# Kernel tuning notes

Measured on AMD Instinct MI355X. Metric: run time of the kernel, lower is better.

## Reference

```python
import jax, jax.numpy as jnp
import numpy as np

B, T, C = 2, 2048, 2048
N_HEAD, N_KV_HEAD = 16, 4
HEAD_DIM = C // N_HEAD  # 128
HALF = HEAD_DIM // 2    # 64


def _rms_norm(x):
    # F.rms_norm with no weight: x / sqrt(mean(x^2) + eps), eps = dtype eps
    eps = jnp.finfo(x.dtype).eps
    return x * jax.lax.rsqrt(jnp.mean(x * x, axis=-1, keepdims=True) + eps)


def _rope_apply(x, cos, sin):
    # x: [B, H, T, Hs]; cos/sin: [1, 1, T, Hs/2]
    x1, x2 = x[..., :HALF], x[..., HALF:]
    return jnp.concatenate([x1 * cos - x2 * sin, x1 * sin + x2 * cos], axis=-1)


def setup_inputs() -> dict:
    key = jax.random.key(0)
    ks = jax.random.split(key, 8)
    x = jax.random.normal(ks[0], (B, T, C), dtype=jnp.float32)
    # real RoPE tables (base 10000), shape [1,1,T,HALF]
    inv_freq = 1.0 / (10000.0 ** (np.arange(0, HALF, dtype=np.float32) / HALF))
    t = np.arange(T, dtype=np.float32)
    ang = np.einsum('t,f->tf', t, inv_freq)
    cos = jnp.asarray(np.cos(ang))[None, None]
    sin = jnp.asarray(np.sin(ang))[None, None]
    s = 0.02
    Wq = jax.random.normal(ks[1], (C, N_HEAD * HEAD_DIM), dtype=jnp.float32) * s
    Wk = jax.random.normal(ks[2], (C, N_KV_HEAD * HEAD_DIM), dtype=jnp.float32) * s
    Wv = jax.random.normal(ks[3], (C, N_KV_HEAD * HEAD_DIM), dtype=jnp.float32) * s
    Wo = jax.random.normal(ks[4], (C, C), dtype=jnp.float32) * s
    bo = jnp.zeros((C,), dtype=jnp.float32)
    return {"x": x, "cos": cos, "sin": sin, "Wq": Wq, "Wk": Wk, "Wv": Wv, "Wo": Wo, "bo": bo}


def reference(x, cos, sin, Wq, Wk, Wv, Wo, bo):
    Bq, Tq, Cq = x.shape
    G = N_HEAD // N_KV_HEAD
    # QKV projections (GQA, no bias)
    q = (x @ Wq).reshape(Bq, Tq, N_HEAD, HEAD_DIM)
    k = (x @ Wk).reshape(Bq, Tq, N_KV_HEAD, HEAD_DIM)
    v = (x @ Wv).reshape(Bq, Tq, N_KV_HEAD, HEAD_DIM)
    # QK RMSNorm (over head_dim), then to [B, H, T, Hs]
    q = jnp.transpose(_rms_norm(q), (0, 2, 1, 3))
    k = jnp.transpose(_rms_norm(k), (0, 2, 1, 3))
    v = jnp.transpose(v, (0, 2, 1, 3))
    # RoPE
    q = _rope_apply(q, cos[:, :, :Tq, :], sin[:, :, :Tq, :])
    k = _rope_apply(k, cos[:, :, :Tq, :], sin[:, :, :Tq, :])
    # GQA: repeat kv heads across groups
    k = jnp.repeat(k, G, axis=1)  # [B, H, T, Hs]
    v = jnp.repeat(v, G, axis=1)
    # Causal SDPA
    scale = 1.0 / jnp.sqrt(jnp.asarray(HEAD_DIM, dtype=x.dtype))
    scores = jnp.einsum('bhqd,bhkd->bhqk', q, k) * scale
    causal = jnp.tril(jnp.ones((Tq, Tq), dtype=bool))
    scores = jnp.where(causal, scores, jnp.asarray(-jnp.inf, dtype=scores.dtype))
    attn = jax.nn.softmax(scores, axis=-1)
    y = jnp.einsum('bhqk,bhkd->bhqd', attn, v)
    y = jnp.transpose(y, (0, 2, 1, 3)).reshape(Bq, Tq, Cq)
    return y @ Wo + bo
```

## Files before the change

kernel.cpp:

```cpp
#include <hip/hip_runtime.h>
#include <hip/hip_bf16.h>
#include <math.h>

#define BB 2
#define TT 2048
#define CC 2048
#define NH 16
#define NKV 4
#define HD 128
#define HALF 64
#define MTOT (BB*TT)
#define NQKV (CC + 2*NKV*HD)

typedef unsigned short u16;
typedef __attribute__((ext_vector_type(8))) short bf16x8;
typedef __attribute__((ext_vector_type(4))) float f32x4;

__device__ __forceinline__ u16 f2bf(float f) {
  unsigned u = __float_as_uint(f);
  unsigned r = (u + 0x7FFFu + ((u >> 16) & 1u)) >> 16;
  return (u16)r;
}
__device__ __forceinline__ u16 f2bf_hw(float f) {
  __hip_bfloat16 h = __float2bfloat16(f);
  return *reinterpret_cast<const u16*>(&h);
}
__device__ __forceinline__ float bf2f(u16 v) {
  return __uint_as_float(((unsigned)v) << 16);
}

__device__ __forceinline__ void gl_lds16(const void* g, void* l) {
  __builtin_amdgcn_global_load_lds(
      (const __attribute__((address_space(1))) unsigned int*)g,
      (__attribute__((address_space(3))) unsigned int*)l, 16, 0, 0);
}

__global__ __launch_bounds__(256) void prep(
    const float* __restrict__ x, const float* __restrict__ Wq,
    const float* __restrict__ Wk, const float* __restrict__ Wv,
    const float* __restrict__ Wo, u16* __restrict__ xb,
    u16* __restrict__ Wt, u16* __restrict__ Wot) {
  const int z = blockIdx.z;
  const int tx = threadIdx.x, ty = threadIdx.y;
  if (z == 4) {
    const int tid = ty * 32 + tx;
    const int i = (blockIdx.y * 64 + blockIdx.x) * 256 + tid;
    const float4* s4 = (const float4*)x;
    float4 a = s4[(size_t)i * 2], b = s4[(size_t)i * 2 + 1];
    bf16x8 o;
    o[0] = (short)f2bf(a.x); o[1] = (short)f2bf(a.y);
    o[2] = (short)f2bf(a.z); o[3] = (short)f2bf(a.w);
    o[4] = (short)f2bf(b.x); o[5] = (short)f2bf(b.y);
    o[6] = (short)f2bf(b.z); o[7] = (short)f2bf(b.w);
    ((bf16x8*)xb)[i] = o;
    return;
  }
  const float* W; u16* dst; int N; int row_off;
  if (z == 0)      { W = Wq; dst = Wt;  N = 2048; row_off = 0; }
  else if (z == 1) { W = Wk; dst = Wt;  N = 512;  row_off = 2048; }
  else if (z == 2) { W = Wv; dst = Wt;  N = 512;  row_off = 2560; }
  else             { W = Wo; dst = Wot; N = 2048; row_off = 0; }
  const int n0 = blockIdx.x * 32, k0 = blockIdx.y * 32;
  if (n0 >= N) return;
  __shared__ float tile[32][33];
#pragma unroll
  for (int i = 0; i < 4; ++i)
    tile[ty + 8 * i][tx] = W[(size_t)(k0 + ty + 8 * i) * N + n0 + tx];
  __syncthreads();
#pragma unroll
  for (int i = 0; i < 4; ++i)
    dst[(size_t)(row_off + n0 + ty + 8 * i) * CC + k0 + tx] =
        f2bf(tile[tx][ty + 8 * i]);
}

__global__ __launch_bounds__(512, 2) void gemm_8ph(
    const u16* __restrict__ A, const u16* __restrict__ Bt,
    const float* __restrict__ bias, float* __restrict__ C,
    int M, int N, int K, int out_bf16) {
  __shared__ u16 As[32768];
  __shared__ u16 Bs[32768];
  const int tid = threadIdx.x;
  const int w = tid >> 6, lane = tid & 63;
  const int quad = lane >> 4, lo = lane & 15;
  const int wm = w >> 2, wn = w & 3;
  const int bm = blockIdx.y * 256, bn = blockIdx.x * 256;
  const int NT = K >> 6;

  const u16* agp[2][2]; const u16* bgp[2][2];
#pragma unroll
  for (int h = 0; h < 2; ++h)
#pragma unroll
    for (int j = 0; j < 2; ++j) {
      const unsigned X = (unsigned)h * 16384u +
                         (unsigned)((w * 2 + j) * 64 + lane) * 16u;
      const int row = (int)(X >> 7);
      const int ce = (int)(((X & 127u) ^ (((X >> 7) & 7u) << 4)) >> 1);
      agp[h][j] = A  + (size_t)(bm + row) * K + ce;
      bgp[h][j] = Bt + (size_t)(bn + row) * K + ce;
    }
  char* const lAs = (char*)As;
  char* const lBs = (char*)Bs;
  const int woff = w * 2048;

#define STGA(hh, bufp, kt) do { \
    gl_lds16(agp[hh][0] + (size_t)(kt) * 64, lAs + (bufp) * 32768 + (hh) * 16384 + woff); \
    gl_lds16(agp[hh][1] + (size_t)(kt) * 64, lAs + (bufp) * 32768 + (hh) * 16384 + woff + 1024); \
  } while (0)
#define STGB(hh, bufp, kt) do { \
    gl_lds16(bgp[hh][0] + (size_t)(kt) * 64, lBs + (bufp) * 32768 + (hh) * 16384 + woff); \
    gl_lds16(bgp[hh][1] + (size_t)(kt) * 64, lBs + (bufp) * 32768 + (hh) * 16384 + woff + 1024); \
  } while (0)

  const int sw  = (lo & 7) << 4;
  const int co0 = (quad * 16) ^ sw;
  const int co1 = (64 + quad * 16) ^ sw;
  const int aRB = (wm * 128 + lo) * 128;
  const int bRB = (wn * 64 + lo) * 128;

  f32x4 acc[8][4];
#pragma unroll
  for (int ri = 0; ri < 8; ++ri)
#pragma unroll
    for (int ci = 0; ci < 4; ++ci)
#pragma unroll
      for (int r = 0; r < 4; ++r) acc[ri][ci][r] = 0.f;

  STGA(0, 0, 0); STGA(1, 0, 0); STGB(0, 0, 0); STGB(1, 0, 0);
  STGB(0, 1, 1); STGB(1, 1, 1); STGA(0, 1, 1);
  asm volatile("s_waitcnt vmcnt(6)" ::: "memory");
  __builtin_amdgcn_s_barrier();

  for (int t = 0; t < NT; ++t) {
    const int pa = t & 1;
    const char* Ab = lAs + pa * 32768 + aRB;
    const char* Bb = lBs + pa * 32768 + bRB;
    bf16x8 a[4][2], b0[2][2], b1[2][2];

#pragma unroll
    for (int i = 0; i < 4; ++i) {
      a[i][0] = *(const bf16x8*)(Ab + i * 2048 + co0);
      a[i][1] = *(const bf16x8*)(Ab + i * 2048 + co1);
    }
#pragma unroll
    for (int j = 0; j < 2; ++j) {
      b0[j][0] = *(const bf16x8*)(Bb + j * 2048 + co0);
      b0[j][1] = *(const bf16x8*)(Bb + j * 2048 + co1);
    }
    if (t + 1 < NT) STGA(1, (t + 1) & 1, t + 1);
    __builtin_amdgcn_s_barrier();
    asm volatile("s_waitcnt lgkmcnt(0)");
    __builtin_amdgcn_s_setprio(1);
#pragma unroll
    for (int i = 0; i < 4; ++i)
#pragma unroll
      for (int j = 0; j < 2; ++j) {
        acc[i][j] = __builtin_amdgcn_mfma_f32_16x16x32_bf16(a[i][0], b0[j][0], acc[i][j], 0, 0, 0);
        acc[i][j] = __builtin_amdgcn_mfma_f32_16x16x32_bf16(a[i][1], b0[j][1], acc[i][j], 0, 0, 0);
      }
    __builtin_amdgcn_s_setprio(0);
    __builtin_amdgcn_s_barrier();

#pragma unroll
    for (int j = 0; j < 2; ++j) {
      b1[j][0] = *(const bf16x8*)(Bb + 4096 + j * 2048 + co0);
      b1[j][1] = *(const bf16x8*)(Bb + 4096 + j * 2048 + co1);
    }
    __builtin_amdgcn_s_barrier();
    asm volatile("s_waitcnt lgkmcnt(0)");
    __builtin_amdgcn_s_setprio(1);
#pragma unroll
    for (int i = 0; i < 4; ++i)
#pragma unroll
      for (int j = 0; j < 2; ++j) {
        acc[i][2 + j] = __builtin_amdgcn_mfma_f32_16x16x32_bf16(a[i][0], b1[j][0], acc[i][2 + j], 0, 0, 0);
        acc[i][2 + j] = __builtin_amdgcn_mfma_f32_16x16x32_bf16(a[i][1], b1[j][1], acc[i][2 + j], 0, 0, 0);
      }
    __builtin_amdgcn_s_setprio(0);
    __builtin_amdgcn_s_barrier();

#pragma unroll
    for (int i = 0; i < 4; ++i) {
      a[i][0] = *(const bf16x8*)(Ab + 8192 + i * 2048 + co0);
      a[i][1] = *(const bf16x8*)(Ab + 8192 + i * 2048 + co1);
    }
    if (t + 2 < NT) STGB(0, pa, t + 2);
    __builtin_amdgcn_s_barrier();
    asm volatile("s_waitcnt lgkmcnt(0)");
    __builtin_amdgcn_s_setprio(1);
#pragma unroll
    for (int i = 0; i < 4; ++i)
#pragma unroll
      for (int j = 0; j < 2; ++j) {
        acc[4 + i][2 + j] = __builtin_amdgcn_mfma_f32_16x16x32_bf16(a[i][0], b1[j][0], acc[4 + i][2 + j], 0, 0, 0);
        acc[4 + i][2 + j] = __builtin_amdgcn_mfma_f32_16x16x32_bf16(a[i][1], b1[j][1], acc[4 + i][2 + j], 0, 0, 0);
      }
    __builtin_amdgcn_s_setprio(0);
    __builtin_amdgcn_s_barrier();

    if (t + 2 < NT) { STGB(1, pa, t + 2); STGA(0, pa, t + 2); }
    if (t + 2 < NT)      asm volatile("s_waitcnt vmcnt(6)" ::: "memory");
    else if (t + 1 < NT) asm volatile("s_waitcnt vmcnt(0)" ::: "memory");
    __builtin_amdgcn_s_barrier();
    asm volatile("s_waitcnt lgkmcnt(0)");
    __builtin_amdgcn_s_setprio(1);
#pragma unroll
    for (int i = 0; i < 4; ++i)
#pragma unroll
      for (int j = 0; j < 2; ++j) {
        acc[4 + i][j] = __builtin_amdgcn_mfma_f32_16x16x32_bf16(a[i][0], b0[j][0], acc[4 + i][j], 0, 0, 0);
        acc[4 + i][j] = __builtin_amdgcn_mfma_f32_16x16x32_bf16(a[i][1], b0[j][1], acc[4 + i][j], 0, 0, 0);
      }
    __builtin_amdgcn_s_setprio(0);
    __builtin_amdgcn_s_barrier();
  }
#undef STGA
#undef STGB

  const int rbase = bm + wm * 128;
  const int cbase = bn + wn * 64;
#pragma unroll
  for (int ri = 0; ri < 8; ++ri)
#pragma unroll
    for (int ci = 0; ci < 4; ++ci) {
      const int col = cbase + ci * 16 + lo;
      const float bv = bias ? bias[col] : 0.f;
#pragma unroll
      for (int r = 0; r < 4; ++r) {
        const int row = rbase + ri * 16 + quad * 4 + r;
        const float v = acc[ri][ci][r] + bv;
        if (out_bf16) ((u16*)C)[(size_t)row * N + col] = f2bf(v);
        else          C[(size_t)row * N + col] = v;
      }
    }
}

__global__ __launch_bounds__(512, 2) void gemm_n128(
    const u16* __restrict__ A, const u16* __restrict__ Bt,
    const float* __restrict__ bias, float* __restrict__ C,
    int M, int N, int K, int out_bf16) {
  __shared__ u16 As[32768];
  __shared__ u16 Bs[16384];
  const int tid = threadIdx.x;
  const int w = tid >> 6, lane = tid & 63;
  const int quad = lane >> 4, lo = lane & 15;
  const int wm = w >> 1, wn = w & 1;
  const int bm = blockIdx.y * 256, bn = blockIdx.x * 128;
  const int NT = K >> 6;

  const u16* agp[2][2];
#pragma unroll
  for (int h = 0; h < 2; ++h)
#pragma unroll
    for (int j = 0; j < 2; ++j) {
      const unsigned X = (unsigned)h * 16384u +
                         (unsigned)((w * 2 + j) * 64 + lane) * 16u;
      const int row = (int)(X >> 7);
      const int ce = (int)(((X & 127u) ^ (((X >> 7) & 7u) << 4)) >> 1);
      agp[h][j] = A + (size_t)(bm + row) * K + ce;
    }
  const u16* bgp[2];
#pragma unroll
  for (int j = 0; j < 2; ++j) {
    const unsigned X = (unsigned)((w * 2 + j) * 64 + lane) * 16u;
    const int row = (int)(X >> 7);
    const int ce = (int)(((X & 127u) ^ (((X >> 7) & 7u) << 4)) >> 1);
    bgp[j] = Bt + (size_t)(bn + row) * K + ce;
  }
  char* const lAs = (char*)As;
  char* const lBs = (char*)Bs;
  const int woff = w * 2048;

#define STGA_(hh, bufp, kt) do { \
    gl_lds16(agp[hh][0] + (size_t)(kt) * 64, lAs + (bufp) * 32768 + (hh) * 16384 + woff); \
    gl_lds16(agp[hh][1] + (size_t)(kt) * 64, lAs + (bufp) * 32768 + (hh) * 16384 + woff + 1024); \
  } while (0)
#define STGB_(bufp, kt) do { \
    gl_lds16(bgp[0] + (size_t)(kt) * 64, lBs + (bufp) * 16384 + woff); \
    gl_lds16(bgp[1] + (size_t)(kt) * 64, lBs + (bufp) * 16384 + woff + 1024); \
  } while (0)

  const int sw  = (lo & 7) << 4;
  const int co0 = (quad * 16) ^ sw;
  const int co1 = (64 + quad * 16) ^ sw;
  const int aRB = (wm * 64 + lo) * 128;
  const int bRB = (wn * 64 + lo) * 128;

  f32x4 acc[4][4];
#pragma unroll
  for (int i = 0; i < 4; ++i)
#pragma unroll
    for (int ci = 0; ci < 4; ++ci)
#pragma unroll
      for (int r = 0; r < 4; ++r) acc[i][ci][r] = 0.f;

  STGA_(0, 0, 0); STGA_(1, 0, 0); STGB_(0, 0);
  STGB_(1, 1); STGA_(0, 1, 1);
  asm volatile("s_waitcnt vmcnt(4)" ::: "memory");
  __builtin_amdgcn_s_barrier();

  for (int t = 0; t < NT; ++t) {
    const int pa = t & 1;
    const char* Ab = lAs + pa * 32768 + aRB;
    const char* Bb = lBs + pa * 16384 + bRB;
    bf16x8 a[4][2], b[4][2];
#pragma unroll
    for (int i = 0; i < 4; ++i) {
      a[i][0] = *(const bf16x8*)(Ab + i * 2048 + co0);
      a[i][1] = *(const bf16x8*)(Ab + i * 2048 + co1);
    }
#pragma unroll
    for (int ci = 0; ci < 4; ++ci) {
      b[ci][0] = *(const bf16x8*)(Bb + ci * 2048 + co0);
      b[ci][1] = *(const bf16x8*)(Bb + ci * 2048 + co1);
    }
    if (t + 1 < NT) STGA_(1, (t + 1) & 1, t + 1);
    asm volatile("s_waitcnt lgkmcnt(0)");
    __builtin_amdgcn_s_barrier();
    __builtin_amdgcn_s_setprio(1);
#pragma unroll
    for (int i = 0; i < 4; ++i)
#pragma unroll
      for (int ci = 0; ci < 2; ++ci) {
        acc[i][ci] = __builtin_amdgcn_mfma_f32_16x16x32_bf16(a[i][0], b[ci][0], acc[i][ci], 0, 0, 0);
        acc[i][ci] = __builtin_amdgcn_mfma_f32_16x16x32_bf16(a[i][1], b[ci][1], acc[i][ci], 0, 0, 0);
      }
    __builtin_amdgcn_s_setprio(0);
    if (t + 2 < NT) { STGB_(pa, t + 2); STGA_(0, pa, t + 2); }
    if (t + 2 < NT)      asm volatile("s_waitcnt vmcnt(4)" ::: "memory");
    else if (t + 1 < NT) asm volatile("s_waitcnt vmcnt(0)" ::: "memory");
    __builtin_amdgcn_s_setprio(1);
#pragma unroll
    for (int i = 0; i < 4; ++i)
#pragma unroll
      for (int ci = 2; ci < 4; ++ci) {
        acc[i][ci] = __builtin_amdgcn_mfma_f32_16x16x32_bf16(a[i][0], b[ci][0], acc[i][ci], 0, 0, 0);
        acc[i][ci] = __builtin_amdgcn_mfma_f32_16x16x32_bf16(a[i][1], b[ci][1], acc[i][ci], 0, 0, 0);
      }
    __builtin_amdgcn_s_setprio(0);
    __builtin_amdgcn_s_barrier();
  }
#undef STGA_
#undef STGB_

  const int rbase = bm + wm * 64;
  const int cbase = bn + wn * 64;
#pragma unroll
  for (int i = 0; i < 4; ++i)
#pragma unroll
    for (int ci = 0; ci < 4; ++ci) {
      const int col = cbase + ci * 16 + lo;
      const float bv = bias ? bias[col] : 0.f;
#pragma unroll
      for (int r = 0; r < 4; ++r) {
        const int row = rbase + i * 16 + quad * 4 + r;
        const float v = acc[i][ci][r] + bv;
        if (out_bf16) ((u16*)C)[(size_t)row * N + col] = f2bf(v);
        else          C[(size_t)row * N + col] = v;
      }
    }
}

__global__ __launch_bounds__(256) void qkv_post(
    const u16* __restrict__ qkv_lin, const float* __restrict__ cosp,
    const float* __restrict__ sinp, u16* __restrict__ q, u16* __restrict__ k,
    u16* __restrict__ vt) {
  __shared__ u16 tile[32][33];
  if (blockIdx.y == 5) {
    const int bx = blockIdx.x;
    if (bx >= 2048) return;
    const int t0 = (bx & 63) * 32, d0 = ((bx >> 6) & 3) * 32;
    const int p = bx >> 8;
    const int b = p >> 2, kv = p & 3;
    const int tx = threadIdx.x & 31, ty = threadIdx.x >> 5;
#pragma unroll
    for (int i = 0; i < 4; ++i)
      tile[ty + 8 * i][tx] =
          qkv_lin[(size_t)(b * TT + t0 + ty + 8 * i) * NQKV + CC + NKV * HD + kv * HD + d0 + tx];
    __syncthreads();
    const int tperm = ((tx >> 2) & 3) * 8 + (tx & 3) + 4 * ((tx >> 4) & 1);
#pragma unroll
    for (int i = 0; i < 4; ++i)
      vt[((size_t)p * HD + d0 + ty + 8 * i) * TT + t0 + tperm] = tile[tx][ty + 8 * i];
    return;
  }
  const int bt = blockIdx.x;
  const int hh = blockIdx.y * 4 + (threadIdx.x >> 6);
  const int lane = threadIdx.x & 63;
  const int t = bt & (TT - 1), b = bt >> 11;
  const int col = (hh < NH) ? hh * HD : CC + (hh - NH) * HD;
  const u16* src = qkv_lin + (size_t)bt * NQKV + col;
  float v1 = bf2f(src[lane]), v2 = bf2f(src[lane + 64]);
  float ss = v1 * v1 + v2 * v2;
#pragma unroll
  for (int mm = 1; mm < 64; mm <<= 1) ss += __shfl_xor(ss, mm, 64);
  float rms = rsqrtf(ss * (1.f / 128.f) + 1.1920929e-7f);
  float c = cosp[t * HALF + lane], s = sinp[t * HALF + lane];
  float o1 = v1 * rms * c - v2 * rms * s;
  float o2 = v1 * rms * s + v2 * rms * c;
  if (hh < NH) {
    u16* dst = q + (((size_t)(b * NH + hh)) * TT + t) * HD;
    dst[lane] = f2bf(o1); dst[lane + 64] = f2bf(o2);
  } else {
    u16* dst = k + (((size_t)(b * NKV + (hh - NH))) * TT + t) * HD;
    dst[lane] = f2bf(o1); dst[lane + 64] = f2bf(o2);
  }
}

__device__ __forceinline__ void softmax_pack(
    const f32x4* sacc, float& l_lane, bf16x8* ap, int rowq, int t0,
    bool diag, int quad) {
  const float cc = 0.12751744050808612f;
  float e[4][4];
  if (diag) {
#pragma unroll
    for (int ct = 0; ct < 4; ++ct)
#pragma unroll
      for (int r = 0; r < 4; ++r) {
        float v = __builtin_amdgcn_exp2f(sacc[ct][r] * cc);
        if (t0 + ct * 16 + quad * 4 + r > rowq) v = 0.f;
        l_lane += v; e[ct][r] = v;
      }
  } else {
#pragma unroll
    for (int ct = 0; ct < 4; ++ct)
#pragma unroll
      for (int r = 0; r < 4; ++r) {
        float v = __builtin_amdgcn_exp2f(sacc[ct][r] * cc);
        l_lane += v; e[ct][r] = v;
      }
  }
#pragma unroll
  for (int k2 = 0; k2 < 2; ++k2) {
    bf16x8 ch;
#pragma unroll
    for (int j = 0; j < 8; ++j)
      ch[j] = (short)f2bf_hw(e[k2 * 2 + (j >> 2)][j & 3]);
    ap[k2] = ch;
  }
}

__global__ __launch_bounds__(512, 4) void attn_mfma(
    const u16* __restrict__ Qb, const u16* __restrict__ Kb,
    const u16* __restrict__ Vt, u16* __restrict__ Y) {
  __shared__ u16 Ks[2][8192];
  __shared__ u16 Vs[2][8192];

  const int qt = blockIdx.x;
  const int bh = blockIdx.y;
  const int b = bh >> 4, h = bh & 15, kvh = h >> 2;
  const int tid = threadIdx.x;
  const int wave = tid >> 6, lane = tid & 63;
  const int wg = wave >> 2, wv = wave & 3;
  const int quad = lane >> 4, lo = lane & 15;

  const int rows = (wg == 0) ? qt * 64 : (31 - qt) * 64;
  const u16* Qg = Qb + (size_t)(b * NH + h) * TT * HD;
  const u16* Kg = Kb + (size_t)(b * NKV + kvh) * TT * HD;
  const u16* Vg = Vt + (size_t)(b * NKV + kvh) * HD * TT;

  bf16x8 aq[4];
#pragma unroll
  for (int kc = 0; kc < 4; ++kc)
    aq[kc] = *(const bf16x8*)(Qg + (size_t)(rows + wv * 16 + lo) * HD + kc * 32 + quad * 8);

  const u16* kgp[2]; const u16* vgp[2];
  u16* klp[2][2]; u16* vlp[2][2];
#pragma unroll
  for (int c = 0; c < 2; ++c) {
    const int s = wave * 2 + c;
    const int ct = s >> 2, kq = s & 3;
    kgp[c] = Kg + (size_t)(ct * 16 + lo) * HD + kq * 32 + quad * 8;
    const int dt = s >> 1, k2 = s & 1;
    vgp[c] = Vg + (size_t)(dt * 16 + lo) * TT + k2 * 32 + quad * 8;
    klp[0][c] = &Ks[0][s * 512]; klp[1][c] = &Ks[1][s * 512];
    vlp[0][c] = &Vs[0][s * 512]; vlp[1][c] = &Vs[1][s * 512];
  }

  f32x4 oacc[8];
#pragma unroll
  for (int dt = 0; dt < 8; ++dt)
#pragma unroll
    for (int r = 0; r < 4; ++r) oacc[dt][r] = 0.f;
  float l_lane = 0.f;

  const int ntiles = 32 - qt;
  const int rowq = rows + wv * 16 + lo;

#pragma unroll
  for (int c = 0; c < 2; ++c) {
    gl_lds16(kgp[c], klp[0][c]); kgp[c] += 64 * HD;
    gl_lds16(vgp[c], vlp[0][c]); vgp[c] += 64;
  }

  for (int nt = 0; nt < ntiles; ++nt) {
    const int par = nt & 1;
    __syncthreads();
    if (nt + 1 < ntiles) {
#pragma unroll
      for (int c = 0; c < 2; ++c) {
        gl_lds16(kgp[c], klp[par ^ 1][c]); kgp[c] += 64 * HD;
        gl_lds16(vgp[c], vlp[par ^ 1][c]); vgp[c] += 64;
      }
    }
    const bool act = (wg == 1) || (nt <= qt);
    if (act) {
      const u16* ksb = Ks[par];
      const u16* vsb = Vs[par];
      const int t0 = nt * 64;

      f32x4 sacc[4];
#pragma unroll
      for (int ct = 0; ct < 4; ++ct)
#pragma unroll
        for (int r = 0; r < 4; ++r) sacc[ct][r] = 0.f;
      __builtin_amdgcn_s_setprio(1);
#pragma unroll
      for (int ct = 0; ct < 4; ++ct)
#pragma unroll
        for (int kc = 0; kc < 4; ++kc) {
          bf16x8 bk = *(const bf16x8*)&ksb[(ct * 4 + kc) * 512 + lane * 8];
          sacc[ct] = __builtin_amdgcn_mfma_f32_16x16x32_bf16(bk, aq[kc], sacc[ct], 0, 0, 0);
        }
      __builtin_amdgcn_s_setprio(0);

      bf16x8 ap[2];
      softmax_pack(sacc, l_lane, ap, rowq, t0, t0 + 63 > rows + wv * 16, quad);

      __builtin_amdgcn_s_setprio(1);
#pragma unroll
      for (int dt = 0; dt < 8; ++dt)
#pragma unroll
        for (int k2 = 0; k2 < 2; ++k2) {
          bf16x8 bv = *(const bf16x8*)&vsb[(dt * 2 + k2) * 512 + lane * 8];
          oacc[dt] = __builtin_amdgcn_mfma_f32_16x16x32_bf16(ap[k2], bv, oacc[dt], 0, 0, 0);
        }
      __builtin_amdgcn_s_setprio(0);
    }
  }

  float l = l_lane;
  l += __shfl_xor(l, 16, 64);
  l += __shfl_xor(l, 32, 64);
  l = 1.f / l;
  float linv[4];
#pragma unroll
  for (int r = 0; r < 4; ++r)
    linv[r] = __shfl(l, quad * 4 + r, 64);
  const size_t row0 = (size_t)b * TT + rows + wv * 16 + quad * 4;
#pragma unroll
  for (int dt = 0; dt < 8; ++dt)
#pragma unroll
    for (int r = 0; r < 4; ++r)
      Y[(row0 + r) * CC + h * HD + dt * 16 + lo] = f2bf(oacc[dt][r] * linv[r]);
}

extern "C" void kernel_launch(void* const* d_in, const int* in_sizes, int n_in,
                              void* d_out, int out_size, void* d_ws, size_t ws_size,
                              hipStream_t stream) {
  (void)in_sizes; (void)n_in; (void)out_size; (void)ws_size;
  const float* x    = (const float*)d_in[0];
  const float* cosp = (const float*)d_in[1];
  const float* sinp = (const float*)d_in[2];
  const float* Wq   = (const float*)d_in[3];
  const float* Wk   = (const float*)d_in[4];
  const float* Wv   = (const float*)d_in[5];
  const float* Wo   = (const float*)d_in[6];
  const float* bo   = (const float*)d_in[7];
  float* out = (float*)d_out;
  char* ws = (char*)d_ws;

  const size_t MB = 1024 * 1024;
  u16* xb      = (u16*)(ws);
  u16* Wt      = (u16*)(ws + 16 * MB);
  u16* qkv_lin = (u16*)(ws + 28 * MB);
  u16* Wot     = (u16*)(ws + 52 * MB);
  u16* qb_buf  = (u16*)(ws);
  u16* kb      = (u16*)(ws + 16 * MB);
  u16* vt      = (u16*)(ws + 20 * MB);
  u16* y       = (u16*)(ws + 28 * MB);

  prep<<<dim3(64, 64, 5), dim3(32, 8), 0, stream>>>(x, Wq, Wk, Wv, Wo, xb, Wt, Wot);

  gemm_8ph<<<dim3(NQKV / 256, MTOT / 256), 512, 0, stream>>>(
      xb, Wt, nullptr, (float*)qkv_lin, MTOT, NQKV, CC, 1);

  qkv_post<<<dim3(MTOT, 6), 256, 0, stream>>>(qkv_lin, cosp, sinp, qb_buf, kb, vt);

  attn_mfma<<<dim3(16, BB * NH), 512, 0, stream>>>(qb_buf, kb, vt, y);

  gemm_n128<<<dim3(CC / 128, MTOT / 256), 512, 0, stream>>>(
      y, Wot, bo, out, MTOT, CC, CC, 0);
}
```

Measured before the change: 304.4 us.

## Add XCD-aware block swizzle to GEMMs and vectorize RMSNorm/RoPE loads

Both GEMM kernels remap the linear workgroup id so that consecutive tiles land on the same XCD, aiming for better L2 reuse of A/B tiles across neighbouring blocks. The norm/RoPE kernel now loads and stores bf16 pairs as 32-bit words and uses cross-lane shuffles to fetch the rotation partner, which cuts the number of memory transactions. The swizzle assumes the grid size is divisible by 8, and the shuffles add some ALU work.

```diff
diff --git a/kernel.cpp b/kernel.cpp
--- a/kernel.cpp
+++ b/kernel.cpp
@@ -33,6 +33,10 @@
   __builtin_amdgcn_global_load_lds(
       (const __attribute__((address_space(1))) unsigned int*)g,
       (__attribute__((address_space(3))) unsigned int*)l, 16, 0, 0);
+}
+
+__device__ __forceinline__ int xcd_swz(int bid, int nwg) {
+  return (bid & 7) * (nwg >> 3) + (bid >> 3);
 }
 
 __global__ __launch_bounds__(256) void prep(
@@ -83,7 +87,9 @@
   const int w = tid >> 6, lane = tid & 63;
   const int quad = lane >> 4, lo = lane & 15;
   const int wm = w >> 2, wn = w & 3;
-  const int bm = blockIdx.y * 256, bn = blockIdx.x * 256;
+  const int nwg = gridDim.x * gridDim.y;
+  const int swz = xcd_swz(blockIdx.y * gridDim.x + blockIdx.x, nwg);
+  const int bm = (swz / gridDim.x) * 256, bn = (swz % gridDim.x) * 256;
   const int NT = K >> 6;
 
   const u16* agp[2][2]; const u16* bgp[2][2];
@@ -244,7 +250,9 @@
   const int w = tid >> 6, lane = tid & 63;
   const int quad = lane >> 4, lo = lane & 15;
   const int wm = w >> 1, wn = w & 1;
-  const int bm = blockIdx.y * 256, bn = blockIdx.x * 128;
+  const int nwg = gridDim.x * gridDim.y;
+  const int swz = xcd_swz(blockIdx.y * gridDim.x + blockIdx.x, nwg);
+  const int bm = (swz / gridDim.x) * 256, bn = (swz % gridDim.x) * 128;
   const int NT = K >> 6;
 
   const u16* agp[2][2];
@@ -386,24 +394,35 @@
   const int bt = blockIdx.x;
   const int hh = blockIdx.y * 4 + (threadIdx.x >> 6);
   const int lane = threadIdx.x & 63;
+  const int lam = lane & 31;
   const int t = bt & (TT - 1), b = bt >> 11;
   const int col = (hh < NH) ? hh * HD : CC + (hh - NH) * HD;
   const u16* src = qkv_lin + (size_t)bt * NQKV + col;
-  float v1 = bf2f(src[lane]), v2 = bf2f(src[lane + 64]);
-  float ss = v1 * v1 + v2 * v2;
+  const unsigned wv = *(const unsigned*)(src + 2 * lane);
+  const float e0 = bf2f((u16)(wv & 0xFFFFu)), e1 = bf2f((u16)(wv >> 16));
+  float ss = e0 * e0 + e1 * e1;
 #pragma unroll
   for (int mm = 1; mm < 64; mm <<= 1) ss += __shfl_xor(ss, mm, 64);
-  float rms = rsqrtf(ss * (1.f / 128.f) + 1.1920929e-7f);
-  float c = cosp[t * HALF + lane], s = sinp[t * HALF + lane];
-  float o1 = v1 * rms * c - v2 * rms * s;
-  float o2 = v1 * rms * s + v2 * rms * c;
-  if (hh < NH) {
-    u16* dst = q + (((size_t)(b * NH + hh)) * TT + t) * HD;
-    dst[lane] = f2bf(o1); dst[lane + 64] = f2bf(o2);
+  const float rms = rsqrtf(ss * (1.f / 128.f) + 1.1920929e-7f);
+  const unsigned w1 = (unsigned)__shfl((int)wv, lam, 64);
+  const unsigned w2 = (unsigned)__shfl((int)wv, lam + 32, 64);
+  const float x1a = bf2f((u16)(w1 & 0xFFFFu)), x1b = bf2f((u16)(w1 >> 16));
+  const float x2a = bf2f((u16)(w2 & 0xFFFFu)), x2b = bf2f((u16)(w2 >> 16));
+  const float2 cs = *(const float2*)(cosp + t * HALF + 2 * lam);
+  const float2 sn = *(const float2*)(sinp + t * HALF + 2 * lam);
+  float oa, ob;
+  if (lane < 32) {
+    oa = x1a * rms * cs.x - x2a * rms * sn.x;
+    ob = x1b * rms * cs.y - x2b * rms * sn.y;
   } else {
-    u16* dst = k + (((size_t)(b * NKV + (hh - NH))) * TT + t) * HD;
-    dst[lane] = f2bf(o1); dst[lane + 64] = f2bf(o2);
-  }
+    oa = x1a * rms * sn.x + x2a * rms * cs.x;
+    ob = x1b * rms * sn.y + x2b * rms * cs.y;
+  }
+  const unsigned ow = (unsigned)f2bf(oa) | ((unsigned)f2bf(ob) << 16);
+  u16* dst = (hh < NH)
+      ? q + (((size_t)(b * NH + hh)) * TT + t) * HD
+      : k + (((size_t)(b * NKV + (hh - NH))) * TT + t) * HD;
+  *(unsigned*)(dst + 2 * lane) = ow;
 }
 
 __device__ __forceinline__ void softmax_pack(
```

New measurement: 310.0 us. No clear change (+1.8%).
